# Kernel tuning notes

Hardware: AMD Instinct MI355X
Metric: run time of the kernel (lower is better)

Reference implementation:

```python
import jax, jax.numpy as jnp
import numpy as np

N = 10000      # nodes
E = 320000     # edges (avg degree 32)
H = 64         # hidden_nf
D = 3          # num_dims
L = 4          # n_layers
IN_NODE = 1
IN_EDGE = 2
CEMB = 16      # class_embedding_dim
FH = 32        # field_hidden_size


def setup_inputs() -> dict:
    key = jax.random.key(0)
    ks = iter(jax.random.split(key, 64))
    def nrm(shape, scale=0.05):
        return jax.random.normal(next(ks), shape, dtype=jnp.float32) * scale
    def zeros(shape):
        return jnp.zeros(shape, dtype=jnp.float32)
    inp = {
        # forward args
        "h": nrm((N, IN_NODE), 1.0),
        "x": nrm((N, D), 1.0),
        "vel": nrm((N, D), 1.0),
        "edge_attr": nrm((E, IN_EDGE), 1.0),
        "edges": jax.random.randint(next(ks), (2, E), 0, N, dtype=jnp.int32),
        "charges": jax.random.randint(next(ks), (N,), 0, 2, dtype=jnp.int32),
        # node embedding Linear(in_node_nf, hidden_nf)
        "emb_W": nrm((IN_NODE, H)), "emb_b": zeros((H,)),
        # FieldNetwork: Embedding(2, 16) + MLP(2*D+16 -> 32 -> 32 -> D), SiLU
        "cls_emb": nrm((2, CEMB)),
        "f_W1": nrm((2 * D + CEMB, FH)), "f_b1": zeros((FH,)),
        "f_W2": nrm((FH, FH)), "f_b2": zeros((FH,)),
        "f_W3": nrm((FH, D)), "f_b3": zeros((D,)),
        # per-layer E_GCL_vel_field params, stacked on leading layer dim L
        # edge_mlp: (2H + 1 radial + in_edge_nf) -> H -> H, SiLU after both
        "e_W1": nrm((L, 2 * H + 1 + IN_EDGE, H)), "e_b1": zeros((L, H)),
        "e_W2": nrm((L, H, H)), "e_b2": zeros((L, H)),
        # node_mlp: (H + H) -> H -> H, SiLU only after first
        "n_W1": nrm((L, 2 * H, H)), "n_b1": zeros((L, H)),
        "n_W2": nrm((L, H, H)), "n_b2": zeros((L, H)),
        # coord_mlp: H -> H -> 1 (last layer bias-free, small xavier init)
        "c_W1": nrm((L, H, H)), "c_b1": zeros((L, H)),
        "c_W2": nrm((L, H, 1), 0.001),
        # coord_mlp_vel: H -> H -> 1
        "v_W1": nrm((L, H, H)), "v_b1": zeros((L, H)),
        "v_W2": nrm((L, H, 1)), "v_b2": zeros((L, 1)),
        # coord_mlp_field: H -> H -> 1 (field gating, Aether extension)
        "g_W1": nrm((L, H, H)), "g_b1": zeros((L, H)),
        "g_W2": nrm((L, H, 1)), "g_b2": zeros((L, 1)),
    }
    return inp


def _egnn_forward(h, x, vel, edge_attr, emb_W, emb_b, cls_emb,
                  f_W1, f_b1, f_W2, f_b2, f_W3, f_b3,
                  e_W1, e_b1, e_W2, e_b2, n_W1, n_b1, n_W2, n_b2,
                  c_W1, c_b1, c_W2, v_W1, v_b1, v_W2, v_b2,
                  g_W1, g_b1, g_W2, g_b2, edges, charges):
    row, col = edges[0], edges[1]
    # FieldNetwork: field(pos, vel, charge_class) -> [N, D]
    finp = jnp.concatenate([x, vel, cls_emb[charges]], axis=-1)   # [N, 2D+CEMB]
    fh = jax.nn.silu(finp @ f_W1 + f_b1)
    fh = jax.nn.silu(fh @ f_W2 + f_b2)
    field = fh @ f_W3 + f_b3                                       # [N, D]

    hh = h @ emb_W + emb_b                                         # [N, H]
    coord = x
    ones_e = jnp.ones((E, 1), dtype=x.dtype)
    for i in range(L):
        # coord2radial
        diff = coord[row] - coord[col]                             # [E, D]
        radial = jnp.sum(diff * diff, axis=-1, keepdims=True)      # [E, 1]
        # edge model (gather + MLP)
        e_in = jnp.concatenate([hh[row], hh[col], radial, edge_attr], axis=-1)
        m = jax.nn.silu(e_in @ e_W1[i] + e_b1[i])
        m = jax.nn.silu(m @ e_W2[i] + e_b2[i])                     # [E, H]
        # coord model: mean-aggregate weighted diffs (coords_weight = 1.0)
        cw = jax.nn.silu(m @ c_W1[i] + c_b1[i]) @ c_W2[i]          # [E, 1]
        trans = diff * cw
        csum = jax.ops.segment_sum(trans, row, num_segments=N)     # [N, D]
        cnt = jax.ops.segment_sum(ones_e, row, num_segments=N)     # [N, 1]
        coord = coord + csum / jnp.maximum(cnt, 1.0)
        # velocity and field terms
        vw = jax.nn.silu(hh @ v_W1[i] + v_b1[i]) @ v_W2[i] + v_b2[i]   # [N,1]
        gw = jax.nn.silu(hh @ g_W1[i] + g_b1[i]) @ g_W2[i] + g_b2[i]   # [N,1]
        coord = coord + vw * vel + gw * field
        # node model (scatter-sum messages + MLP)
        magg = jax.ops.segment_sum(m, row, num_segments=N)         # [N, H]
        n_in = jnp.concatenate([hh, magg], axis=-1)
        hh = jax.nn.silu(n_in @ n_W1[i] + n_b1[i]) @ n_W2[i] + n_b2[i]
    return coord


def reference(h, x, vel, edge_attr, edges, charges, emb_W, emb_b, cls_emb,
              f_W1, f_b1, f_W2, f_b2, f_W3, f_b3,
              e_W1, e_b1, e_W2, e_b2, n_W1, n_b1, n_W2, n_b2,
              c_W1, c_b1, c_W2, v_W1, v_b1, v_W2, v_b2,
              g_W1, g_b1, g_W2, g_b2):
    return _egnn_forward(h, x, vel, edge_attr, emb_W, emb_b, cls_emb,
                         f_W1, f_b1, f_W2, f_b2, f_W3, f_b3,
                         e_W1, e_b1, e_W2, e_b2, n_W1, n_b1, n_W2, n_b2,
                         c_W1, c_b1, c_W2, v_W1, v_b1, v_W2, v_b2,
                         g_W1, g_b1, g_W2, g_b2, edges, charges)
```

## Files before the change

### kernel.cpp

```cpp
#include <hip/hip_runtime.h>
#include <hip/hip_bf16.h>

typedef unsigned short ushort_t;
typedef unsigned int uint_t;

#define NN    10000
#define NE    320000
#define NL    4
#define EBLK  64
#define NEBLK 5000
#define NPB   64
#define NNODEBLK 157
#define NPB2  16
#define NODEBLK2 625

#define OFF_FIELD 0
#define OFF_HH    30000
#define OFF_CSUM  670000
#define OFF_MAGG  700000
#define IOFF_CNTI   0
#define IOFF_OFF    10000
#define IOFF_CURSOR 20001
#define IOFF_PERM   30001
#define IOFF_PRER   350004
#define IOFF_PREC   670004

__device__ __forceinline__ float silu(float x) {
    return x * __builtin_amdgcn_rcpf(1.0f + __expf(-x));
}

typedef __fp16 half2v __attribute__((ext_vector_type(2)));
typedef __fp16 f16x8 __attribute__((ext_vector_type(8)));
typedef float f32x4 __attribute__((ext_vector_type(4)));
union U4H8 { uint4 u; f16x8 h; };
__device__ __forceinline__ half2v u2h(uint_t u) {
    union { uint_t u; half2v h; } x; x.u = u; return x.h;
}
__device__ __forceinline__ uint_t h2u(half2v h) {
    union { half2v h; uint_t u; } x; x.h = h; return x.u;
}
__device__ __forceinline__ half2v pkrtz(float a, float b) {
    return __builtin_amdgcn_cvt_pkrtz(a, b);
}
__device__ __forceinline__ float dot2h(half2v a, uint_t w, float c) {
#if __has_builtin(__builtin_amdgcn_fdot2)
    return __builtin_amdgcn_fdot2(a, u2h(w), c, false);
#else
    union { uint_t u; __fp16 h[2]; } x; x.u = w;
    return c + (float)a.x * (float)x.h[0] + (float)a.y * (float)x.h[1];
#endif
}
__device__ __forceinline__ ushort_t f2hbits(float f) {
    union { __fp16 h; ushort_t u; } x; x.h = (__fp16)f; return x.u;
}

__global__ __launch_bounds__(256) void counti_kernel(const int* __restrict__ rows,
                                                     int* __restrict__ cnti) {
    const int e = blockIdx.x * 256 + threadIdx.x;
    if (e < NE) {
        int r = rows[e];
        r = ((uint_t)r < (uint_t)NN) ? r : 0;
        atomicAdd(&cnti[r], 1);
    }
}

__global__ __launch_bounds__(1024) void scan_kernel(const int* __restrict__ cnti,
                                                    int* __restrict__ off,
                                                    int* __restrict__ cursor) {
    __shared__ int part[1024];
    const int t = threadIdx.x;
    const int base = t * 10;
    int loc[10];
    int s = 0;
    #pragma unroll
    for (int i = 0; i < 10; i++) {
        const int idx = base + i;
        const int v = (idx < NN) ? cnti[idx] : 0;
        loc[i] = s; s += v;
    }
    part[t] = s;
    __syncthreads();
    const int own = s;
    for (int d = 1; d < 1024; d <<= 1) {
        const int v = (t >= d) ? part[t - d] : 0;
        __syncthreads();
        part[t] += v;
        __syncthreads();
    }
    const int excl = part[t] - own;
    #pragma unroll
    for (int i = 0; i < 10; i++) {
        const int idx = base + i;
        if (idx < NN) { const int o = excl + loc[i]; off[idx] = o; cursor[idx] = o; }
    }
    if (t == 0) off[NN] = NE;
}

__global__ __launch_bounds__(256) void scatter_kernel(const int* __restrict__ rows,
                                                      int* __restrict__ cursor,
                                                      int* __restrict__ perm) {
    const int e = blockIdx.x * 256 + threadIdx.x;
    if (e < NE) {
        int r = rows[e];
        r = ((uint_t)r < (uint_t)NN) ? r : 0;
        const int pos = atomicAdd(&cursor[r], 1);
        if ((uint_t)pos < (uint_t)NE) perm[pos] = e;
    }
}

__global__ __launch_bounds__(256) void node_init(
    const float* __restrict__ hsrc, const float* __restrict__ xsrc,
    const float* __restrict__ vsrc, const int* __restrict__ charges,
    const float* __restrict__ cls,
    const float* __restrict__ fW1, const float* __restrict__ fb1,
    const float* __restrict__ fW2, const float* __restrict__ fb2,
    const float* __restrict__ fW3, const float* __restrict__ fb3,
    const float* __restrict__ embW, const float* __restrict__ embb,
    float* __restrict__ coord, float* __restrict__ field, float* __restrict__ hh)
{
    __shared__ float sFW1[704], sFW2[1024], sFW3[96];
    __shared__ float sFB1[32], sFB2[32], sFB3[3], sCLS[32], sEW[64], sEB[64];
    const int t = threadIdx.x;
    for (int i = t; i < 704; i += 256) sFW1[i] = fW1[i];
    for (int i = t; i < 1024; i += 256) sFW2[i] = fW2[i];
    if (t < 96) sFW3[t] = fW3[t];
    if (t < 32) { sFB1[t] = fb1[t]; sFB2[t] = fb2[t]; sCLS[t] = cls[t]; }
    if (t < 3)  sFB3[t] = fb3[t];
    if (t < 64) { sEW[t] = embW[t]; sEB[t] = embb[t]; }
    __syncthreads();

    const int n = blockIdx.x * 256 + t;
    if (n >= NN) return;

    float fin[22];
    #pragma unroll
    for (int d = 0; d < 3; d++) {
        fin[d]     = xsrc[3 * n + d];
        fin[3 + d] = vsrc[3 * n + d];
        coord[3 * n + d] = fin[d];
    }
    int ci = charges[n];
    ci = ((uint_t)ci < 2u) ? ci : 0;
    const int cix = ci * 16;
    #pragma unroll
    for (int k = 0; k < 16; k++) fin[6 + k] = sCLS[cix + k];

    float h1[32];
    #pragma unroll
    for (int j = 0; j < 32; j++) h1[j] = sFB1[j];
    #pragma unroll
    for (int k = 0; k < 22; k++) {
        const float v = fin[k];
        #pragma unroll
        for (int j = 0; j < 32; j++) h1[j] += v * sFW1[k * 32 + j];
    }
    #pragma unroll
    for (int j = 0; j < 32; j++) h1[j] = silu(h1[j]);

    float h2[32];
    #pragma unroll
    for (int j = 0; j < 32; j++) h2[j] = sFB2[j];
    #pragma unroll
    for (int k = 0; k < 32; k++) {
        const float v = h1[k];
        #pragma unroll
        for (int j = 0; j < 32; j++) h2[j] += v * sFW2[k * 32 + j];
    }
    #pragma unroll
    for (int j = 0; j < 32; j++) h2[j] = silu(h2[j]);

    #pragma unroll
    for (int d = 0; d < 3; d++) {
        float s = sFB3[d];
        #pragma unroll
        for (int j = 0; j < 32; j++) s += h2[j] * sFW3[j * 3 + d];
        field[3 * n + d] = s;
    }

    const float hv = hsrc[n];
    #pragma unroll
    for (int j = 0; j < 64; j++) hh[(size_t)n * 64 + j] = hv * sEW[j] + sEB[j];
}

__global__ __launch_bounds__(256, 4) void pre_kernel(
    const float* __restrict__ hh,
    const float* __restrict__ gEW1, const float* __restrict__ gEB1,
    uint_t* __restrict__ preR, uint_t* __restrict__ preC)
{
    __shared__ __align__(16) uint_t sW1p[4096];
    __shared__ float sB1[64];
    const int t = threadIdx.x;
    for (int i = t; i < 1024; i += 256) {
        const int kp = i >> 4, j4 = i & 15;
        const float4 w0 = ((const float4*)gEW1)[kp * 32 + j4];
        const float4 w1 = ((const float4*)gEW1)[kp * 32 + 16 + j4];
        uint4 u;
        u.x = h2u(pkrtz(w0.x, w1.x)); u.y = h2u(pkrtz(w0.y, w1.y));
        u.z = h2u(pkrtz(w0.z, w1.z)); u.w = h2u(pkrtz(w0.w, w1.w));
        ((uint4*)sW1p)[i] = u;
    }
    if (t < 64) sB1[t] = gEB1[t];
    __syncthreads();

    const int ni = t >> 2, q = t & 3;
    int n = blockIdx.x * NPB + ni;
    const bool valid = (n < NN);
    n = valid ? n : (NN - 1);
    const float4* h4p = (const float4*)(hh + (size_t)n * 64);

    float acc[16];
    #pragma unroll
    for (int j = 0; j < 16; j++) acc[j] = sB1[q * 16 + j];
    #pragma unroll
    for (int kk = 0; kk < 16; kk++) {
        const float4 a = h4p[kk];
        const half2v p0 = pkrtz(a.x, a.y);
        const half2v p1 = pkrtz(a.z, a.w);
        const uint4* w0 = (const uint4*)&sW1p[(2 * kk) * 64 + q * 16];
        const uint4* w1 = (const uint4*)&sW1p[(2 * kk + 1) * 64 + q * 16];
        #pragma unroll
        for (int j4 = 0; j4 < 4; j4++) {
            const uint4 wa = w0[j4], wb = w1[j4];
            acc[4*j4+0] = dot2h(p1, wb.x, dot2h(p0, wa.x, acc[4*j4+0]));
            acc[4*j4+1] = dot2h(p1, wb.y, dot2h(p0, wa.y, acc[4*j4+1]));
            acc[4*j4+2] = dot2h(p1, wb.z, dot2h(p0, wa.z, acc[4*j4+2]));
            acc[4*j4+3] = dot2h(p1, wb.w, dot2h(p0, wa.w, acc[4*j4+3]));
        }
    }
    if (valid) {
        uint4 o0, o1;
        o0.x = h2u(pkrtz(acc[0],  acc[1]));  o0.y = h2u(pkrtz(acc[2],  acc[3]));
        o0.z = h2u(pkrtz(acc[4],  acc[5]));  o0.w = h2u(pkrtz(acc[6],  acc[7]));
        o1.x = h2u(pkrtz(acc[8],  acc[9]));  o1.y = h2u(pkrtz(acc[10], acc[11]));
        o1.z = h2u(pkrtz(acc[12], acc[13])); o1.w = h2u(pkrtz(acc[14], acc[15]));
        uint4* dst = (uint4*)(preR + (size_t)n * 32 + q * 8);
        dst[0] = o0; dst[1] = o1;
    }

    #pragma unroll
    for (int j = 0; j < 16; j++) acc[j] = 0.f;
    #pragma unroll
    for (int kk = 0; kk < 16; kk++) {
        const float4 a = h4p[kk];
        const half2v p0 = pkrtz(a.x, a.y);
        const half2v p1 = pkrtz(a.z, a.w);
        const uint4* w0 = (const uint4*)&sW1p[(32 + 2 * kk) * 64 + q * 16];
        const uint4* w1 = (const uint4*)&sW1p[(33 + 2 * kk) * 64 + q * 16];
        #pragma unroll
        for (int j4 = 0; j4 < 4; j4++) {
            const uint4 wa = w0[j4], wb = w1[j4];
            acc[4*j4+0] = dot2h(p1, wb.x, dot2h(p0, wa.x, acc[4*j4+0]));
            acc[4*j4+1] = dot2h(p1, wb.y, dot2h(p0, wa.y, acc[4*j4+1]));
            acc[4*j4+2] = dot2h(p1, wb.z, dot2h(p0, wa.z, acc[4*j4+2]));
            acc[4*j4+3] = dot2h(p1, wb.w, dot2h(p0, wa.w, acc[4*j4+3]));
        }
    }
    if (valid) {
        uint4 o0, o1;
        o0.x = h2u(pkrtz(acc[0],  acc[1]));  o0.y = h2u(pkrtz(acc[2],  acc[3]));
        o0.z = h2u(pkrtz(acc[4],  acc[5]));  o0.w = h2u(pkrtz(acc[6],  acc[7]));
        o1.x = h2u(pkrtz(acc[8],  acc[9]));  o1.y = h2u(pkrtz(acc[10], acc[11]));
        o1.z = h2u(pkrtz(acc[12], acc[13])); o1.w = h2u(pkrtz(acc[14], acc[15]));
        uint4* dst = (uint4*)(preC + (size_t)n * 32 + q * 8);
        dst[0] = o0; dst[1] = o1;
    }
}

__global__ __launch_bounds__(256, 6) void edge_kernel(
    const int* __restrict__ rows, const int* __restrict__ cols,
    const int* __restrict__ perm,
    const float* __restrict__ coord,
    const float* __restrict__ eattr,
    const float* __restrict__ gEW1,
    const float* __restrict__ gEW2, const float* __restrict__ gEB2,
    const float* __restrict__ gCW1, const float* __restrict__ gCB1,
    const float* __restrict__ gCW2,
    const uint_t* __restrict__ preR, const uint_t* __restrict__ preC,
    float* __restrict__ csum, float* __restrict__ magg)
{
    __shared__ __align__(16) uint_t tileh[EBLK * 32];
    __shared__ __align__(16) uint_t sWp[2048];
    __shared__ float sExtW[3 * 64];
    __shared__ float sB2[64], sCB1[64], sCW2v[64];
    __shared__ float scw[EBLK];
    __shared__ int   sr[EBLK], sc[EBLK], se[EBLK];
    __shared__ int   segstart[EBLK + 1];
    __shared__ int   snseg;

    const int t = threadIdx.x;
    const int bid = blockIdx.x;
    const int lb  = (bid & 7) * (NEBLK / 8) + (bid >> 3);

    uint4 cwr0, cwr1;
    {
        const int i0 = t, i1 = t + 256;
        const float4 a0 = ((const float4*)gCW1)[(i0 >> 4) * 32 + (i0 & 15)];
        const float4 b0 = ((const float4*)gCW1)[(i0 >> 4) * 32 + 16 + (i0 & 15)];
        cwr0.x = h2u(pkrtz(a0.x, b0.x)); cwr0.y = h2u(pkrtz(a0.y, b0.y));
        cwr0.z = h2u(pkrtz(a0.z, b0.z)); cwr0.w = h2u(pkrtz(a0.w, b0.w));
        const float4 a1 = ((const float4*)gCW1)[(i1 >> 4) * 32 + (i1 & 15)];
        const float4 b1 = ((const float4*)gCW1)[(i1 >> 4) * 32 + 16 + (i1 & 15)];
        cwr1.x = h2u(pkrtz(a1.x, b1.x)); cwr1.y = h2u(pkrtz(a1.y, b1.y));
        cwr1.z = h2u(pkrtz(a1.z, b1.z)); cwr1.w = h2u(pkrtz(a1.w, b1.w));
    }

    for (int i = t; i < 512; i += 256) {
        const int kp = i >> 4, j4 = i & 15;
        const float4 w0 = ((const float4*)gEW2)[kp * 32 + j4];
        const float4 w1 = ((const float4*)gEW2)[kp * 32 + 16 + j4];
        uint4 u;
        u.x = h2u(pkrtz(w0.x, w1.x)); u.y = h2u(pkrtz(w0.y, w1.y));
        u.z = h2u(pkrtz(w0.z, w1.z)); u.w = h2u(pkrtz(w0.w, w1.w));
        ((uint4*)sWp)[i] = u;
    }
    if (t < 192) sExtW[t] = gEW1[8192 + t];
    if (t < 64) { sB2[t] = gEB2[t]; sCB1[t] = gCB1[t]; sCW2v[t] = gCW2[t]; }

    if (t < EBLK) {
        int e = perm[lb * EBLK + t];
        e = ((uint_t)e < (uint_t)NE) ? e : 0;
        int r = rows[e], c = cols[e];
        r = ((uint_t)r < (uint_t)NN) ? r : 0;
        c = ((uint_t)c < (uint_t)NN) ? c : 0;
        se[t] = e; sr[t] = r; sc[t] = c;
    }
    __syncthreads();

    if (t < EBLK) {
        const int flag = (t == 0) ? 1 : ((sr[t] != sr[t - 1]) ? 1 : 0);
        int isc = flag;
        #pragma unroll
        for (int d = 1; d < EBLK; d <<= 1) {
            const int up = __shfl_up(isc, d);
            if (t >= d) isc += up;
        }
        if (flag) segstart[isc - 1] = t;
        if (t == EBLK - 1) { snseg = isc; segstart[isc] = EBLK; }
    }
    __syncthreads();
    const int nseg = snseg;

    const int ei = t >> 2;
    const int q  = t & 3;
    const int swz = ei & 31;
    const int r = sr[ei], c = sc[ei], e = se[ei];

    const float dx = coord[3 * r + 0] - coord[3 * c + 0];
    const float dy = coord[3 * r + 1] - coord[3 * c + 1];
    const float dz = coord[3 * r + 2] - coord[3 * c + 2];
    const float radial = dx * dx + dy * dy + dz * dz;
    const float2 ea = ((const float2*)eattr)[e];

    union { uint4 v[2]; uint_t a[8]; } R, C;
    {
        const uint4* pr = (const uint4*)(preR + (size_t)r * 32);
        const uint4* pc = (const uint4*)(preC + (size_t)c * 32);
        R.v[0] = pr[q * 2]; R.v[1] = pr[q * 2 + 1];
        C.v[0] = pc[q * 2]; C.v[1] = pc[q * 2 + 1];
    }
    float acc16[16];
    #pragma unroll
    for (int p = 0; p < 8; p++) {
        const half2v hr = u2h(R.a[p]);
        const half2v hc = u2h(C.a[p]);
        acc16[2 * p]     = (float)hr.x + (float)hc.x;
        acc16[2 * p + 1] = (float)hr.y + (float)hc.y;
    }
    {
        const float ext3[3] = {radial, ea.x, ea.y};
        #pragma unroll
        for (int x = 0; x < 3; x++) {
            const float v = ext3[x];
            const float* w = &sExtW[x * 64 + q * 16];
            #pragma unroll
            for (int j = 0; j < 16; j++) acc16[j] += v * w[j];
        }
    }
    #pragma unroll
    for (int j = 0; j < 16; j++) acc16[j] = silu(acc16[j]);
    #pragma unroll
    for (int p = 0; p < 8; p++)
        tileh[ei * 32 + ((q * 8 + p) ^ swz)] = h2u(pkrtz(acc16[2 * p], acc16[2 * p + 1]));
    __syncthreads();

    const int lane = t & 63;
    const int wv   = t >> 6;
    const int lrow = lane & 15;
    const int lkg  = lane >> 4;
    const int arow = wv * 16 + lrow;
    const int aswz = arow & 31;

    U4H8 a0, a1;
    {
        const int kb0 = lkg * 4;
        a0.u.x = tileh[arow * 32 + ((kb0 + 0) ^ aswz)];
        a0.u.y = tileh[arow * 32 + ((kb0 + 1) ^ aswz)];
        a0.u.z = tileh[arow * 32 + ((kb0 + 2) ^ aswz)];
        a0.u.w = tileh[arow * 32 + ((kb0 + 3) ^ aswz)];
        const int kb1 = 16 + lkg * 4;
        a1.u.x = tileh[arow * 32 + ((kb1 + 0) ^ aswz)];
        a1.u.y = tileh[arow * 32 + ((kb1 + 1) ^ aswz)];
        a1.u.z = tileh[arow * 32 + ((kb1 + 2) ^ aswz)];
        a1.u.w = tileh[arow * 32 + ((kb1 + 3) ^ aswz)];
    }

    f32x4 accn[4];
    #pragma unroll
    for (int n = 0; n < 4; n++) {
        const float b = sB2[n * 16 + lrow];
        f32x4 v = {b, b, b, b};
        accn[n] = v;
    }
    #pragma unroll
    for (int n = 0; n < 4; n++) {
        const int bc = n * 16 + lrow;
        U4H8 b0, b1;
        b0.u.x = sWp[(lkg * 4 + 0) * 64 + bc];
        b0.u.y = sWp[(lkg * 4 + 1) * 64 + bc];
        b0.u.z = sWp[(lkg * 4 + 2) * 64 + bc];
        b0.u.w = sWp[(lkg * 4 + 3) * 64 + bc];
        b1.u.x = sWp[(16 + lkg * 4 + 0) * 64 + bc];
        b1.u.y = sWp[(16 + lkg * 4 + 1) * 64 + bc];
        b1.u.z = sWp[(16 + lkg * 4 + 2) * 64 + bc];
        b1.u.w = sWp[(16 + lkg * 4 + 3) * 64 + bc];
        accn[n] = __builtin_amdgcn_mfma_f32_16x16x32_f16(a0.h, b0.h, accn[n], 0, 0, 0);
        accn[n] = __builtin_amdgcn_mfma_f32_16x16x32_f16(a1.h, b1.h, accn[n], 0, 0, 0);
    }
    __syncthreads();

    ((uint4*)sWp)[t]       = cwr0;
    ((uint4*)sWp)[t + 256] = cwr1;
    {
        ushort_t* th16 = (ushort_t*)tileh;
        const int mrow = wv * 16 + lkg * 4;
        #pragma unroll
        for (int n = 0; n < 4; n++) {
            const int ch = n * 16 + lrow;
            const int wi = ch >> 1;
            #pragma unroll
            for (int r2 = 0; r2 < 4; r2++) {
                const int edge = mrow + r2;
                th16[(edge * 32 + (wi ^ (edge & 31))) * 2 + (ch & 1)] =
                    f2hbits(silu(accn[n][r2]));
            }
        }
    }
    __syncthreads();

    U4H8 ma0, ma1;
    {
        const int kb0 = lkg * 4;
        ma0.u.x = tileh[arow * 32 + ((kb0 + 0) ^ aswz)];
        ma0.u.y = tileh[arow * 32 + ((kb0 + 1) ^ aswz)];
        ma0.u.z = tileh[arow * 32 + ((kb0 + 2) ^ aswz)];
        ma0.u.w = tileh[arow * 32 + ((kb0 + 3) ^ aswz)];
        const int kb1 = 16 + lkg * 4;
        ma1.u.x = tileh[arow * 32 + ((kb1 + 0) ^ aswz)];
        ma1.u.y = tileh[arow * 32 + ((kb1 + 1) ^ aswz)];
        ma1.u.z = tileh[arow * 32 + ((kb1 + 2) ^ aswz)];
        ma1.u.w = tileh[arow * 32 + ((kb1 + 3) ^ aswz)];
    }
    f32x4 cacc[4];
    #pragma unroll
    for (int n = 0; n < 4; n++) {
        const float b = sCB1[n * 16 + lrow];
        f32x4 v = {b, b, b, b};
        cacc[n] = v;
    }
    #pragma unroll
    for (int n = 0; n < 4; n++) {
        const int bc = n * 16 + lrow;
        U4H8 b0, b1;
        b0.u.x = sWp[(lkg * 4 + 0) * 64 + bc];
        b0.u.y = sWp[(lkg * 4 + 1) * 64 + bc];
        b0.u.z = sWp[(lkg * 4 + 2) * 64 + bc];
        b0.u.w = sWp[(lkg * 4 + 3) * 64 + bc];
        b1.u.x = sWp[(16 + lkg * 4 + 0) * 64 + bc];
        b1.u.y = sWp[(16 + lkg * 4 + 1) * 64 + bc];
        b1.u.z = sWp[(16 + lkg * 4 + 2) * 64 + bc];
        b1.u.w = sWp[(16 + lkg * 4 + 3) * 64 + bc];
        cacc[n] = __builtin_amdgcn_mfma_f32_16x16x32_f16(ma0.h, b0.h, cacc[n], 0, 0, 0);
        cacc[n] = __builtin_amdgcn_mfma_f32_16x16x32_f16(ma1.h, b1.h, cacc[n], 0, 0, 0);
    }
    float p0 = 0.f, p1 = 0.f, p2 = 0.f, p3 = 0.f;
    #pragma unroll
    for (int n = 0; n < 4; n++) {
        const float w2v = sCW2v[n * 16 + lrow];
        p0 += silu(cacc[n][0]) * w2v;
        p1 += silu(cacc[n][1]) * w2v;
        p2 += silu(cacc[n][2]) * w2v;
        p3 += silu(cacc[n][3]) * w2v;
    }
    #pragma unroll
    for (int m = 1; m <= 8; m <<= 1) {
        p0 += __shfl_xor(p0, m);
        p1 += __shfl_xor(p1, m);
        p2 += __shfl_xor(p2, m);
        p3 += __shfl_xor(p3, m);
    }
    if (lrow == 0) {
        const int mrow = wv * 16 + lkg * 4;
        scw[mrow + 0] = p0; scw[mrow + 1] = p1;
        scw[mrow + 2] = p2; scw[mrow + 3] = p3;
    }

    for (int w = t; w < nseg * 64; w += 256) {
        const int lr2 = w >> 6, cc = w & 63;
        const int pp0 = segstart[lr2], pp1 = segstart[lr2 + 1];
        const int kp = cc >> 1, hi = cc & 1;
        float s = 0.f;
        for (int p = pp0; p < pp1; p++) {
            const half2v h = u2h(tileh[p * 32 + (kp ^ (p & 31))]);
            s += hi ? (float)h.y : (float)h.x;
        }
        atomicAdd(&magg[(size_t)sr[pp0] * 64 + cc], s);
    }
    __syncthreads();

    const float cw = scw[ei];
    float* tf = (float*)tileh;
    if (q < 3) tf[ei * 4 + q] = (q == 0 ? dx : (q == 1 ? dy : dz)) * cw;
    __syncthreads();
    for (int w = t; w < nseg * 3; w += 256) {
        const int lr2 = w / 3, cc = w - 3 * lr2;
        const int pp0 = segstart[lr2], pp1 = segstart[lr2 + 1];
        float s = 0.f;
        for (int p = pp0; p < pp1; p++) s += tf[p * 4 + cc];
        atomicAdd(&csum[3 * sr[pp0] + cc], s);
    }
}

__global__ __launch_bounds__(256, 2) void node_kernel(
    const float* __restrict__ gVW1, const float* __restrict__ gVB1,
    const float* __restrict__ gVW2, const float* __restrict__ gVB2,
    const float* __restrict__ gGW1, const float* __restrict__ gGB1,
    const float* __restrict__ gGW2, const float* __restrict__ gGB2,
    const float* __restrict__ gNW1, const float* __restrict__ gNB1,
    const float* __restrict__ gNW2, const float* __restrict__ gNB2,
    const float* __restrict__ gW1n, const float* __restrict__ gB1n,
    float* __restrict__ csum, const int* __restrict__ off,
    const float* __restrict__ vsrc, const float* __restrict__ field,
    float* __restrict__ magg,
    float* __restrict__ coord, float* __restrict__ hh,
    uint_t* __restrict__ preR, uint_t* __restrict__ preC, const int emit_pre)
{
    __shared__ __align__(16) uint_t sNW1p[4096];
    __shared__ __align__(16) uint_t sW1np[4096];
    __shared__ __align__(16) uint_t sVW1p[2048];
    __shared__ __align__(16) uint_t sGW1p[2048];
    __shared__ __align__(16) float sNW2[4096];
    __shared__ __align__(16) float tile[NPB2 * 136];
    __shared__ float sNB1[64], sNB2[64], sB1n[64];

    const int t = threadIdx.x;
    for (int i = t; i < 1024; i += 256) {
        const int kp = i >> 4, j4 = i & 15;
        const float4 w0 = ((const float4*)gNW1)[kp * 32 + j4];
        const float4 w1 = ((const float4*)gNW1)[kp * 32 + 16 + j4];
        uint4 u;
        u.x = h2u(pkrtz(w0.x, w1.x)); u.y = h2u(pkrtz(w0.y, w1.y));
        u.z = h2u(pkrtz(w0.z, w1.z)); u.w = h2u(pkrtz(w0.w, w1.w));
        ((uint4*)sNW1p)[i] = u;
    }
    for (int i = t; i < 1024; i += 256) {
        const int kp = i >> 4, j4 = i & 15;
        const float4 w0 = ((const float4*)gW1n)[kp * 32 + j4];
        const float4 w1 = ((const float4*)gW1n)[kp * 32 + 16 + j4];
        uint4 u;
        u.x = h2u(pkrtz(w0.x, w1.x)); u.y = h2u(pkrtz(w0.y, w1.y));
        u.z = h2u(pkrtz(w0.z, w1.z)); u.w = h2u(pkrtz(w0.w, w1.w));
        ((uint4*)sW1np)[i] = u;
    }
    for (int i = t; i < 512; i += 256) {
        const int kp = i >> 4, j4 = i & 15;
        const float4 w0 = ((const float4*)gVW1)[kp * 32 + j4];
        const float4 w1 = ((const float4*)gVW1)[kp * 32 + 16 + j4];
        uint4 u;
        u.x = h2u(pkrtz(w0.x, w1.x)); u.y = h2u(pkrtz(w0.y, w1.y));
        u.z = h2u(pkrtz(w0.z, w1.z)); u.w = h2u(pkrtz(w0.w, w1.w));
        ((uint4*)sVW1p)[i] = u;
    }
    for (int i = t; i < 512; i += 256) {
        const int kp = i >> 4, j4 = i & 15;
        const float4 w0 = ((const float4*)gGW1)[kp * 32 + j4];
        const float4 w1 = ((const float4*)gGW1)[kp * 32 + 16 + j4];
        uint4 u;
        u.x = h2u(pkrtz(w0.x, w1.x)); u.y = h2u(pkrtz(w0.y, w1.y));
        u.z = h2u(pkrtz(w0.z, w1.z)); u.w = h2u(pkrtz(w0.w, w1.w));
        ((uint4*)sGW1p)[i] = u;
    }
    for (int i = t; i < 1024; i += 256)
        ((float4*)sNW2)[i] = ((const float4*)gNW2)[i];
    if (t < 64) { sNB1[t] = gNB1[t]; sNB2[t] = gNB2[t]; sB1n[t] = gB1n[t]; }

    const int ni = t >> 4;
    const int q  = t & 15;
    const int n = blockIdx.x * NPB2 + ni;
    float* T = &tile[ni * 136];

    ((float4*)T)[q]        = ((const float4*)(hh + (size_t)n * 64))[q];
    ((float4*)(T + 68))[q] = ((const float4*)(magg + (size_t)n * 64))[q];
    __syncthreads();

    float v4[4], g4[4];
    {
        const float4 bv = ((const float4*)gVB1)[q];
        const float4 bg = ((const float4*)gGB1)[q];
        v4[0] = bv.x; v4[1] = bv.y; v4[2] = bv.z; v4[3] = bv.w;
        g4[0] = bg.x; g4[1] = bg.y; g4[2] = bg.z; g4[3] = bg.w;
    }
    #pragma unroll 8
    for (int kp = 0; kp < 32; kp++) {
        const half2v p = pkrtz(T[2 * kp], T[2 * kp + 1]);
        const uint4 wv = *(const uint4*)&sVW1p[kp * 64 + q * 4];
        const uint4 wg = *(const uint4*)&sGW1p[kp * 64 + q * 4];
        v4[0] = dot2h(p, wv.x, v4[0]); v4[1] = dot2h(p, wv.y, v4[1]);
        v4[2] = dot2h(p, wv.z, v4[2]); v4[3] = dot2h(p, wv.w, v4[3]);
        g4[0] = dot2h(p, wg.x, g4[0]); g4[1] = dot2h(p, wg.y, g4[1]);
        g4[2] = dot2h(p, wg.z, g4[2]); g4[3] = dot2h(p, wg.w, g4[3]);
    }
    float partv, partg;
    {
        const float4 wv2 = ((const float4*)gVW2)[q];
        const float4 wg2 = ((const float4*)gGW2)[q];
        partv = silu(v4[0]) * wv2.x + silu(v4[1]) * wv2.y
              + silu(v4[2]) * wv2.z + silu(v4[3]) * wv2.w;
        partg = silu(g4[0]) * wg2.x + silu(g4[1]) * wg2.y
              + silu(g4[2]) * wg2.z + silu(g4[3]) * wg2.w;
    }
    partv += __shfl_xor(partv, 1);  partg += __shfl_xor(partg, 1);
    partv += __shfl_xor(partv, 2);  partg += __shfl_xor(partg, 2);
    partv += __shfl_xor(partv, 4);  partg += __shfl_xor(partg, 4);
    partv += __shfl_xor(partv, 8);  partg += __shfl_xor(partg, 8);
    const float vw = partv + gVB2[0];
    const float gw = partg + gGB2[0];

    if (q == 0) {
        const float cn = fmaxf((float)(off[n + 1] - off[n]), 1.0f);
        #pragma unroll
        for (int d = 0; d < 3; d++)
            coord[3 * n + d] += csum[3 * n + d] / cn
                              + vw * vsrc[3 * n + d]
                              + gw * field[3 * n + d];
    }

    float aA[4], aB[4];
    {
        const float4 b = ((const float4*)sNB1)[q];
        aA[0] = b.x; aA[1] = b.y; aA[2] = b.z; aA[3] = b.w;
        aB[0] = aB[1] = aB[2] = aB[3] = 0.f;
    }
    #pragma unroll 8
    for (int kp = 0; kp < 32; kp++) {
        const half2v pA = pkrtz(T[2 * kp], T[2 * kp + 1]);
        const half2v pB = pkrtz(T[68 + 2 * kp], T[68 + 2 * kp + 1]);
        const uint4 wA = *(const uint4*)&sNW1p[kp * 64 + q * 4];
        const uint4 wB = *(const uint4*)&sNW1p[(32 + kp) * 64 + q * 4];
        aA[0] = dot2h(pA, wA.x, aA[0]); aA[1] = dot2h(pA, wA.y, aA[1]);
        aA[2] = dot2h(pA, wA.z, aA[2]); aA[3] = dot2h(pA, wA.w, aA[3]);
        aB[0] = dot2h(pB, wB.x, aB[0]); aB[1] = dot2h(pB, wB.y, aB[1]);
        aB[2] = dot2h(pB, wB.z, aB[2]); aB[3] = dot2h(pB, wB.w, aB[3]);
    }
    float a4[4];
    #pragma unroll
    for (int j = 0; j < 4; j++) a4[j] = silu(aA[j] + aB[j]);

    __syncthreads();
    {
        float4 v; v.x = a4[0]; v.y = a4[1]; v.z = a4[2]; v.w = a4[3];
        ((float4*)T)[q] = v;
    }
    __syncthreads();

    {
        float4 z; z.x = z.y = z.z = z.w = 0.f;
        ((float4*)(magg + (size_t)n * 64))[q] = z;
        if (q == 0) { csum[3 * n] = 0.f; csum[3 * n + 1] = 0.f; csum[3 * n + 2] = 0.f; }
    }

    float oA[4], oB[4];
    {
        const float4 b = ((const float4*)sNB2)[q];
        oA[0] = b.x; oA[1] = b.y; oA[2] = b.z; oA[3] = b.w;
        oB[0] = oB[1] = oB[2] = oB[3] = 0.f;
    }
    #pragma unroll 4
    for (int kk = 0; kk < 8; kk++) {
        const float4 hA = ((const float4*)T)[2 * kk];
        const float4 hB = ((const float4*)T)[2 * kk + 1];
        const float avA[4] = {hA.x, hA.y, hA.z, hA.w};
        const float avB[4] = {hB.x, hB.y, hB.z, hB.w};
        #pragma unroll
        for (int u = 0; u < 4; u++) {
            const float vA = avA[u];
            const float vB = avB[u];
            const float4 wA = ((const float4*)(sNW2 + (8 * kk + u) * 64))[q];
            const float4 wB = ((const float4*)(sNW2 + (8 * kk + 4 + u) * 64))[q];
            oA[0] += vA * wA.x; oA[1] += vA * wA.y; oA[2] += vA * wA.z; oA[3] += vA * wA.w;
            oB[0] += vB * wB.x; oB[1] += vB * wB.y; oB[2] += vB * wB.z; oB[3] += vB * wB.w;
        }
    }
    float o4[4];
    #pragma unroll
    for (int j = 0; j < 4; j++) o4[j] = oA[j] + oB[j];
    {
        float4 v; v.x = o4[0]; v.y = o4[1]; v.z = o4[2]; v.w = o4[3];
        ((float4*)(hh + (size_t)n * 64))[q] = v;
    }

    if (emit_pre) {
        __syncthreads();
        {
            float4 v; v.x = o4[0]; v.y = o4[1]; v.z = o4[2]; v.w = o4[3];
            ((float4*)T)[q] = v;
        }
        __syncthreads();

        float aR[4], aC[4];
        {
            const float4 b = ((const float4*)sB1n)[q];
            aR[0] = b.x; aR[1] = b.y; aR[2] = b.z; aR[3] = b.w;
            aC[0] = aC[1] = aC[2] = aC[3] = 0.f;
        }
        #pragma unroll 8
        for (int kp = 0; kp < 32; kp++) {
            const half2v p = pkrtz(T[2 * kp], T[2 * kp + 1]);
            const uint4 wr = *(const uint4*)&sW1np[kp * 64 + q * 4];
            const uint4 wc = *(const uint4*)&sW1np[(32 + kp) * 64 + q * 4];
            aR[0] = dot2h(p, wr.x, aR[0]); aR[1] = dot2h(p, wr.y, aR[1]);
            aR[2] = dot2h(p, wr.z, aR[2]); aR[3] = dot2h(p, wr.w, aR[3]);
            aC[0] = dot2h(p, wc.x, aC[0]); aC[1] = dot2h(p, wc.y, aC[1]);
            aC[2] = dot2h(p, wc.z, aC[2]); aC[3] = dot2h(p, wc.w, aC[3]);
        }
        uint2 oR, oC;
        oR.x = h2u(pkrtz(aR[0], aR[1])); oR.y = h2u(pkrtz(aR[2], aR[3]));
        oC.x = h2u(pkrtz(aC[0], aC[1])); oC.y = h2u(pkrtz(aC[2], aC[3]));
        *(uint2*)(preR + (size_t)n * 32 + q * 2) = oR;
        *(uint2*)(preC + (size_t)n * 32 + q * 2) = oC;
    }
}

extern "C" void kernel_launch(void* const* d_in, const int* in_sizes, int n_in,
                              void* d_out, int out_size, void* d_ws, size_t ws_size,
                              hipStream_t stream) {
    float* wsf = (float*)d_ws;
    int*   wsi = (int*)(wsf + 1340000);
    uint_t* preR = (uint_t*)(wsi + IOFF_PRER);
    uint_t* preC = (uint_t*)(wsi + IOFF_PREC);
    float* coord = (float*)d_out;
    const int* edges = (const int*)d_in[4];
    const int* rows = edges;
    const int* cols = edges + NE;

    hipMemsetAsync(wsi + IOFF_CNTI, 0, NN * sizeof(int), stream);
    counti_kernel<<<(NE + 255) / 256, 256, 0, stream>>>(rows, wsi + IOFF_CNTI);
    scan_kernel<<<1, 1024, 0, stream>>>(wsi + IOFF_CNTI, wsi + IOFF_OFF, wsi + IOFF_CURSOR);
    scatter_kernel<<<(NE + 255) / 256, 256, 0, stream>>>(rows, wsi + IOFF_CURSOR,
                                                         wsi + IOFF_PERM);

    node_init<<<(NN + 255) / 256, 256, 0, stream>>>(
        (const float*)d_in[0], (const float*)d_in[1], (const float*)d_in[2],
        (const int*)d_in[5], (const float*)d_in[8],
        (const float*)d_in[9],  (const float*)d_in[10],
        (const float*)d_in[11], (const float*)d_in[12],
        (const float*)d_in[13], (const float*)d_in[14],
        (const float*)d_in[6],  (const float*)d_in[7],
        coord, wsf + OFF_FIELD, wsf + OFF_HH);

    hipMemsetAsync(wsf + OFF_CSUM, 0, (30000 + 640000) * sizeof(float), stream);

    pre_kernel<<<NNODEBLK, 256, 0, stream>>>(
        wsf + OFF_HH,
        (const float*)d_in[15], (const float*)d_in[16],
        preR, preC);

    for (int l = 0; l < NL; l++) {
        const int ln = (l + 1 < NL) ? (l + 1) : 0;
        edge_kernel<<<NEBLK, 256, 0, stream>>>(
            rows, cols, wsi + IOFF_PERM,
            coord, (const float*)d_in[3],
            ((const float*)d_in[15]) + l * 8384,
            ((const float*)d_in[17]) + l * 4096, ((const float*)d_in[18]) + l * 64,
            ((const float*)d_in[23]) + l * 4096, ((const float*)d_in[24]) + l * 64,
            ((const float*)d_in[25]) + l * 64,
            preR, preC,
            wsf + OFF_CSUM, wsf + OFF_MAGG);
        node_kernel<<<NODEBLK2, 256, 0, stream>>>(
            ((const float*)d_in[26]) + l * 4096, ((const float*)d_in[27]) + l * 64,
            ((const float*)d_in[28]) + l * 64,   ((const float*)d_in[29]) + l,
            ((const float*)d_in[30]) + l * 4096, ((const float*)d_in[31]) + l * 64,
            ((const float*)d_in[32]) + l * 64,   ((const float*)d_in[33]) + l,
            ((const float*)d_in[19]) + l * 8192, ((const float*)d_in[20]) + l * 64,
            ((const float*)d_in[21]) + l * 4096, ((const float*)d_in[22]) + l * 64,
            ((const float*)d_in[15]) + ln * 8384, ((const float*)d_in[16]) + ln * 64,
            wsf + OFF_CSUM, wsi + IOFF_OFF, (const float*)d_in[2],
            wsf + OFF_FIELD, wsf + OFF_MAGG, coord, wsf + OFF_HH,
            preR, preC, (l + 1 < NL) ? 1 : 0);
    }
}
```

Measured before the change: 485.7 us.

## Use 16-byte swizzled LDS layouts for edge tile and weights with vector loads

Changes the LDS swizzle for the activation tile and the packed weight matrix from a 4-byte-granularity XOR to a 16-byte-group XOR. The MFMA operand fetches can then be single uint4 loads instead of eight scalar LDS reads each. The weight matrix is stored column-major per output channel so each B fragment is contiguous. It also raises the launch-bounds occupancy hint from 6 to 8 waves, which may force register spilling.

Result: faster. 465.2 us (-4.2%).

```diff
diff --git a/kernel.cpp b/kernel.cpp
--- a/kernel.cpp
+++ b/kernel.cpp
@@ -266,7 +266,7 @@
     }
 }
 
-__global__ __launch_bounds__(256, 6) void edge_kernel(
+__global__ __launch_bounds__(256, 8) void edge_kernel(
     const int* __restrict__ rows, const int* __restrict__ cols,
     const int* __restrict__ perm,
     const float* __restrict__ coord,
@@ -308,10 +308,14 @@
         const int kp = i >> 4, j4 = i & 15;
         const float4 w0 = ((const float4*)gEW2)[kp * 32 + j4];
         const float4 w1 = ((const float4*)gEW2)[kp * 32 + 16 + j4];
-        uint4 u;
-        u.x = h2u(pkrtz(w0.x, w1.x)); u.y = h2u(pkrtz(w0.y, w1.y));
-        u.z = h2u(pkrtz(w0.z, w1.z)); u.w = h2u(pkrtz(w0.w, w1.w));
-        ((uint4*)sWp)[i] = u;
+        const int kg = kp >> 2, kj = kp & 3;
+        const uint_t vals[4] = { h2u(pkrtz(w0.x, w1.x)), h2u(pkrtz(w0.y, w1.y)),
+                                 h2u(pkrtz(w0.z, w1.z)), h2u(pkrtz(w0.w, w1.w)) };
+        #pragma unroll
+        for (int cc = 0; cc < 4; cc++) {
+            const int bc = j4 * 4 + cc;
+            sWp[bc * 32 + ((kg ^ (bc & 7)) << 2) + kj] = vals[cc];
+        }
     }
     if (t < 192) sExtW[t] = gEW1[8192 + t];
     if (t < 64) { sB2[t] = gEB2[t]; sCB1[t] = gCB1[t]; sCW2v[t] = gCW2[t]; }
@@ -342,7 +346,7 @@
 
     const int ei = t >> 2;
     const int q  = t & 3;
-    const int swz = ei & 31;
+    const int e7 = ei & 7;
     const int r = sr[ei], c = sc[ei], e = se[ei];
 
     const float dx = coord[3 * r + 0] - coord[3 * c + 0];
@@ -378,9 +382,15 @@
     }
     #pragma unroll
     for (int j = 0; j < 16; j++) acc16[j] = silu(acc16[j]);
-    #pragma unroll
-    for (int p = 0; p < 8; p++)
-        tileh[ei * 32 + ((q * 8 + p) ^ swz)] = h2u(pkrtz(acc16[2 * p], acc16[2 * p + 1]));
+    {
+        uint4 g0, g1;
+        g0.x = h2u(pkrtz(acc16[0],  acc16[1]));  g0.y = h2u(pkrtz(acc16[2],  acc16[3]));
+        g0.z = h2u(pkrtz(acc16[4],  acc16[5]));  g0.w = h2u(pkrtz(acc16[6],  acc16[7]));
+        g1.x = h2u(pkrtz(acc16[8],  acc16[9]));  g1.y = h2u(pkrtz(acc16[10], acc16[11]));
+        g1.z = h2u(pkrtz(acc16[12], acc16[13])); g1.w = h2u(pkrtz(acc16[14], acc16[15]));
+        ((uint4*)tileh)[ei * 8 + ((q * 2) ^ e7)]     = g0;
+        ((uint4*)tileh)[ei * 8 + ((q * 2 + 1) ^ e7)] = g1;
+    }
     __syncthreads();
 
     const int lane = t & 63;
@@ -388,21 +398,11 @@
     const int lrow = lane & 15;
     const int lkg  = lane >> 4;
     const int arow = wv * 16 + lrow;
-    const int aswz = arow & 31;
+    const int e7a  = arow & 7;
 
     U4H8 a0, a1;
-    {
-        const int kb0 = lkg * 4;
-        a0.u.x = tileh[arow * 32 + ((kb0 + 0) ^ aswz)];
-        a0.u.y = tileh[arow * 32 + ((kb0 + 1) ^ aswz)];
-        a0.u.z = tileh[arow * 32 + ((kb0 + 2) ^ aswz)];
-        a0.u.w = tileh[arow * 32 + ((kb0 + 3) ^ aswz)];
-        const int kb1 = 16 + lkg * 4;
-        a1.u.x = tileh[arow * 32 + ((kb1 + 0) ^ aswz)];
-        a1.u.y = tileh[arow * 32 + ((kb1 + 1) ^ aswz)];
-        a1.u.z = tileh[arow * 32 + ((kb1 + 2) ^ aswz)];
-        a1.u.w = tileh[arow * 32 + ((kb1 + 3) ^ aswz)];
-    }
+    a0.u = ((const uint4*)tileh)[arow * 8 + (lkg ^ e7a)];
+    a1.u = ((const uint4*)tileh)[arow * 8 + ((4 + lkg) ^ e7a)];
 
     f32x4 accn[4];
     #pragma unroll
@@ -414,22 +414,30 @@
     #pragma unroll
     for (int n = 0; n < 4; n++) {
         const int bc = n * 16 + lrow;
+        const int b7 = bc & 7;
         U4H8 b0, b1;
-        b0.u.x = sWp[(lkg * 4 + 0) * 64 + bc];
-        b0.u.y = sWp[(lkg * 4 + 1) * 64 + bc];
-        b0.u.z = sWp[(lkg * 4 + 2) * 64 + bc];
-        b0.u.w = sWp[(lkg * 4 + 3) * 64 + bc];
-        b1.u.x = sWp[(16 + lkg * 4 + 0) * 64 + bc];
-        b1.u.y = sWp[(16 + lkg * 4 + 1) * 64 + bc];
-        b1.u.z = sWp[(16 + lkg * 4 + 2) * 64 + bc];
-        b1.u.w = sWp[(16 + lkg * 4 + 3) * 64 + bc];
+        b0.u = ((const uint4*)sWp)[bc * 8 + (lkg ^ b7)];
+        b1.u = ((const uint4*)sWp)[bc * 8 + ((4 + lkg) ^ b7)];
         accn[n] = __builtin_amdgcn_mfma_f32_16x16x32_f16(a0.h, b0.h, accn[n], 0, 0, 0);
         accn[n] = __builtin_amdgcn_mfma_f32_16x16x32_f16(a1.h, b1.h, accn[n], 0, 0, 0);
     }
     __syncthreads();
 
-    ((uint4*)sWp)[t]       = cwr0;
-    ((uint4*)sWp)[t + 256] = cwr1;
+    {
+        const int kp0 = t >> 4, j4w = t & 15;
+        const int kg0 = kp0 >> 2, kj0 = kp0 & 3;
+        const int kp1 = kp0 + 16;
+        const int kg1 = kp1 >> 2, kj1 = kp1 & 3;
+        const uint_t v0[4] = {cwr0.x, cwr0.y, cwr0.z, cwr0.w};
+        const uint_t v1[4] = {cwr1.x, cwr1.y, cwr1.z, cwr1.w};
+        #pragma unroll
+        for (int cc = 0; cc < 4; cc++) {
+            const int bc = j4w * 4 + cc;
+            const int b7 = bc & 7;
+            sWp[bc * 32 + ((kg0 ^ b7) << 2) + kj0] = v0[cc];
+            sWp[bc * 32 + ((kg1 ^ b7) << 2) + kj1] = v1[cc];
+        }
+    }
     {
         ushort_t* th16 = (ushort_t*)tileh;
         const int mrow = wv * 16 + lkg * 4;
@@ -437,10 +445,11 @@
         for (int n = 0; n < 4; n++) {
             const int ch = n * 16 + lrow;
             const int wi = ch >> 1;
+            const int wg = wi >> 2, wj = wi & 3, hl = ch & 1;
             #pragma unroll
             for (int r2 = 0; r2 < 4; r2++) {
                 const int edge = mrow + r2;
-                th16[(edge * 32 + (wi ^ (edge & 31))) * 2 + (ch & 1)] =
+                th16[(edge * 32 + ((wg ^ (edge & 7)) << 2) + wj) * 2 + hl] =
                     f2hbits(silu(accn[n][r2]));
             }
         }
@@ -448,18 +457,8 @@
     __syncthreads();
 
     U4H8 ma0, ma1;
-    {
-        const int kb0 = lkg * 4;
-        ma0.u.x = tileh[arow * 32 + ((kb0 + 0) ^ aswz)];
-        ma0.u.y = tileh[arow * 32 + ((kb0 + 1) ^ aswz)];
-        ma0.u.z = tileh[arow * 32 + ((kb0 + 2) ^ aswz)];
-        ma0.u.w = tileh[arow * 32 + ((kb0 + 3) ^ aswz)];
-        const int kb1 = 16 + lkg * 4;
-        ma1.u.x = tileh[arow * 32 + ((kb1 + 0) ^ aswz)];
-        ma1.u.y = tileh[arow * 32 + ((kb1 + 1) ^ aswz)];
-        ma1.u.z = tileh[arow * 32 + ((kb1 + 2) ^ aswz)];
-        ma1.u.w = tileh[arow * 32 + ((kb1 + 3) ^ aswz)];
-    }
+    ma0.u = ((const uint4*)tileh)[arow * 8 + (lkg ^ e7a)];
+    ma1.u = ((const uint4*)tileh)[arow * 8 + ((4 + lkg) ^ e7a)];
     f32x4 cacc[4];
     #pragma unroll
     for (int n = 0; n < 4; n++) {
@@ -470,15 +469,10 @@
     #pragma unroll
     for (int n = 0; n < 4; n++) {
         const int bc = n * 16 + lrow;
+        const int b7 = bc & 7;
         U4H8 b0, b1;
-        b0.u.x = sWp[(lkg * 4 + 0) * 64 + bc];
-        b0.u.y = sWp[(lkg * 4 + 1) * 64 + bc];
-        b0.u.z = sWp[(lkg * 4 + 2) * 64 + bc];
-        b0.u.w = sWp[(lkg * 4 + 3) * 64 + bc];
-        b1.u.x = sWp[(16 + lkg * 4 + 0) * 64 + bc];
-        b1.u.y = sWp[(16 + lkg * 4 + 1) * 64 + bc];
-        b1.u.z = sWp[(16 + lkg * 4 + 2) * 64 + bc];
-        b1.u.w = sWp[(16 + lkg * 4 + 3) * 64 + bc];
+        b0.u = ((const uint4*)sWp)[bc * 8 + (lkg ^ b7)];
+        b1.u = ((const uint4*)sWp)[bc * 8 + ((4 + lkg) ^ b7)];
         cacc[n] = __builtin_amdgcn_mfma_f32_16x16x32_f16(ma0.h, b0.h, cacc[n], 0, 0, 0);
         cacc[n] = __builtin_amdgcn_mfma_f32_16x16x32_f16(ma1.h, b1.h, cacc[n], 0, 0, 0);
     }
@@ -508,9 +502,10 @@
         const int lr2 = w >> 6, cc = w & 63;
         const int pp0 = segstart[lr2], pp1 = segstart[lr2 + 1];
         const int kp = cc >> 1, hi = cc & 1;
+        const int kg = kp >> 2, kj = kp & 3;
         float s = 0.f;
         for (int p = pp0; p < pp1; p++) {
-            const half2v h = u2h(tileh[p * 32 + (kp ^ (p & 31))]);
+            const half2v h = u2h(tileh[p * 32 + ((kg ^ (p & 7)) << 2) + kj]);
             s += hi ? (float)h.y : (float)h.x;
         }
         atomicAdd(&magg[(size_t)sr[pp0] * 64 + cc], s);
```
